# Kernel tuning notes

Hardware: AMD Instinct MI355X
Metric: run time of the kernel (lower is better)

## Reference

```python
import jax, jax.numpy as jnp
import numpy as np
from jax import lax

D_MODEL, D_STATE, D_CONV, EXPAND = 1024, 16, 4, 2
D_INNER = EXPAND * D_MODEL
B_SZ, L_SEQ = 2, 2048

# BitLinear quantization (BitNet b1.58 style, STE via stop_gradient)

def _weight_quant(w):
    scale = jnp.maximum(jnp.mean(jnp.abs(w)), 1e-5)
    q = jnp.clip(jnp.round(w / scale), -1.0, 1.0) * scale
    return w + lax.stop_gradient(q - w)

def _act_quant(x):
    s = 127.0 / jnp.maximum(jnp.max(jnp.abs(x), axis=-1, keepdims=True), 1e-5)
    q = jnp.clip(jnp.round(x * s), -128.0, 127.0) / s
    return x + lax.stop_gradient(q - x)

def bitlinear(x, w, b=None):
    y = _act_quant(x) @ _weight_quant(w).T
    return y + b if b is not None else y


def setup_inputs() -> dict:
    key = jax.random.key(0)
    ks = jax.random.split(key, 9)
    inp = {
        "x": jax.random.normal(ks[0], (B_SZ, L_SEQ, D_MODEL), jnp.float32),
        "in_proj_w": jax.random.normal(ks[1], (2 * D_INNER, D_MODEL), jnp.float32) * 0.02,
        "conv_w": jax.random.normal(ks[2], (D_INNER, 1, D_CONV), jnp.float32) * 0.2,
        "conv_b": jnp.zeros((D_INNER,), jnp.float32),
        "delta_w": jax.random.normal(ks[3], (D_STATE, D_INNER), jnp.float32) * 0.02,
        "delta_b": jnp.zeros((D_STATE,), jnp.float32),
        "B_w": jax.random.normal(ks[4], (D_STATE, D_INNER), jnp.float32) * 0.02,
        "C_w": jax.random.normal(ks[5], (D_STATE, D_INNER), jnp.float32) * 0.02,
        "out_w": jax.random.normal(ks[6], (D_MODEL, D_INNER), jnp.float32) * 0.02,
        "D": jnp.ones((D_INNER,), jnp.float32),
        "log_A": -0.5 * jnp.log(1.0 + jnp.arange(1, D_STATE + 1, dtype=jnp.float32) / D_STATE),
    }
    return inp


def reference(x, in_proj_w, conv_w, conv_b, delta_w, delta_b, B_w, C_w, out_w, D, log_A):
    B, L, _ = x.shape
    # input projection + SiLU gating
    xp = bitlinear(x, in_proj_w)                      # [B, L, 2*d_inner]
    x_gate, x_input = jnp.split(xp, 2, axis=-1)
    x_input = jax.nn.silu(x_gate) * x_input          # [B, L, d_inner]
    # causal depthwise conv1d (padding d_conv-1 then truncation == left-pad)
    xc = lax.conv_general_dilated(
        x_input.transpose(0, 2, 1), conv_w, window_strides=(1,),
        padding=[(D_CONV - 1, 0)], feature_group_count=D_INNER)
    x_input = (xc + conv_b[None, :, None]).transpose(0, 2, 1)  # [B, L, d_inner]
    # selective parameters
    delta = bitlinear(x_input, delta_w, delta_b)     # [B, L, N]
    A_d = jnp.exp(delta * log_A[None, None, :])      # [B, L, N]
    B_mat = bitlinear(x_input, B_w)                  # [B, L, N]
    C_mat = bitlinear(x_input, C_w)                  # [B, L, N]
    # diagonal state recurrence via lax.scan over time
    dB = delta * B_mat                               # [B, L, N]
    def step(h, ins):
        a_t, db_t, c_t = ins                         # each [B, N]
        h = a_t * h + db_t
        return h, jnp.sum(c_t * h, axis=-1)          # signal: [B]
    h0 = jnp.zeros((B, D_STATE), x.dtype)
    _, sig = lax.scan(step, h0, (A_d.transpose(1, 0, 2), dB.transpose(1, 0, 2), C_mat.transpose(1, 0, 2)))
    state_signal = sig.T[:, :, None]                 # [B, L, 1]
    y_inner = x_input * (jax.nn.sigmoid(state_signal) + D[None, None, :])
    return bitlinear(y_inner, out_w)                 # [B, L, d_model]
```

## Files before the change

### kernel.cpp

```cpp
#include <hip/hip_runtime.h>
#include <hip/hip_bf16.h>

typedef signed char i8;
typedef int v4i __attribute__((ext_vector_type(4)));

#define LSTR 80

__device__ __forceinline__ void gld16(const void* g, void* l) {
  __builtin_amdgcn_global_load_lds(
      (const __attribute__((address_space(1))) unsigned int*)g,
      (__attribute__((address_space(3))) unsigned int*)l, 16, 0, 0);
}

__global__ __launch_bounds__(256) void k_abssum_all(const float* __restrict__ w0, const float* __restrict__ w1,
                                                    const float* __restrict__ w2, const float* __restrict__ w3,
                                                    const float* __restrict__ w4, double* __restrict__ partial) {
  int b = blockIdx.x;
  const float* w; int n, nb, bg;
  if (b < 256)      { w = w0; n = 4194304; nb = 256; bg = b; }
  else if (b < 272) { w = w1; n = 32768;   nb = 16;  bg = b - 256; }
  else if (b < 288) { w = w2; n = 32768;   nb = 16;  bg = b - 272; }
  else if (b < 304) { w = w3; n = 32768;   nb = 16;  bg = b - 288; }
  else              { w = w4; n = 2097152; nb = 128; bg = b - 304; }
  __shared__ double sd[256];
  double acc = 0.0;
  for (int i = bg * 256 + threadIdx.x; i < n; i += nb * 256) acc += (double)fabsf(w[i]);
  sd[threadIdx.x] = acc;
  __syncthreads();
  for (int s = 128; s > 0; s >>= 1) {
    if (threadIdx.x < s) sd[threadIdx.x] += sd[threadIdx.x + s];
    __syncthreads();
  }
  if (threadIdx.x == 0) partial[b] = sd[0];
}

__global__ void k_finalize(const double* __restrict__ partial, float* __restrict__ scales) {
  int m = threadIdx.x;
  if (m >= 5) return;
  const int off[6] = {0, 256, 272, 288, 304, 432};
  const double cnt[5] = {4194304.0, 32768.0, 32768.0, 32768.0, 2097152.0};
  double s = 0.0;
  for (int i = off[m]; i < off[m + 1]; ++i) s += partial[i];
  scales[m] = fmaxf((float)(s / cnt[m]), 1e-5f);
}

__global__ __launch_bounds__(256) void k_wquant_all(const float* __restrict__ w0, const float* __restrict__ w1,
                                                    const float* __restrict__ w2, const float* __restrict__ w3,
                                                    const float* __restrict__ w4, const float* __restrict__ scales,
                                                    i8* __restrict__ tin, i8* __restrict__ t2, i8* __restrict__ tout) {
  int b = blockIdx.x;
  const float* w; i8* t; int m, n;
  if (b < 4096)      { w = w0; t = tin;          m = 0; n = 4194304; }
  else if (b < 4128) { w = w1; t = t2;           m = 1; n = 32768; b -= 4096; }
  else if (b < 4160) { w = w2; t = t2 + 32768;   m = 2; n = 32768; b -= 4128; }
  else if (b < 4192) { w = w3; t = t2 + 65536;   m = 3; n = 32768; b -= 4160; }
  else               { w = w4; t = tout;         m = 4; n = 2097152; b -= 4192; }
  int idx = (b * 256 + threadIdx.x) * 4;
  if (idx >= n) return;
  float scale = scales[m];
  float4 v = *(const float4*)(w + idx);
  char4 q;
  q.x = (i8)fminf(fmaxf(rintf(v.x / scale), -1.f), 1.f);
  q.y = (i8)fminf(fmaxf(rintf(v.y / scale), -1.f), 1.f);
  q.z = (i8)fminf(fmaxf(rintf(v.z / scale), -1.f), 1.f);
  q.w = (i8)fminf(fmaxf(rintf(v.w / scale), -1.f), 1.f);
  *(char4*)(t + idx) = q;
}

template <int W>
__global__ __launch_bounds__(256) void k_actquant(const float* __restrict__ x,
                                                  i8* __restrict__ q, float* __restrict__ srow) {
  constexpr int E = W / 256;
  const int r = blockIdx.x, tid = threadIdx.x;
  const float* xr = x + (size_t)r * W;
  float v[E];
  float m = 0.f;
#pragma unroll
  for (int j = 0; j < E; j += 4) {
    float4 t = *(const float4*)(xr + tid * E + j);
    v[j] = t.x; v[j + 1] = t.y; v[j + 2] = t.z; v[j + 3] = t.w;
    m = fmaxf(m, fmaxf(fmaxf(fabsf(t.x), fabsf(t.y)), fmaxf(fabsf(t.z), fabsf(t.w))));
  }
  __shared__ float sm[4];
  __shared__ float sbc;
#pragma unroll
  for (int off = 32; off > 0; off >>= 1) m = fmaxf(m, __shfl_xor(m, off));
  if ((tid & 63) == 0) sm[tid >> 6] = m;
  __syncthreads();
  if (tid == 0) {
    float mm = fmaxf(fmaxf(sm[0], sm[1]), fmaxf(sm[2], sm[3]));
    float s = 127.0f / fmaxf(mm, 1e-5f);
    sbc = s;
    srow[r] = s;
  }
  __syncthreads();
  float s = sbc;
#pragma unroll
  for (int j = 0; j < E; j += 4) {
    char4 c;
    c.x = (i8)fminf(fmaxf(rintf(v[j] * s), -128.f), 127.f);
    c.y = (i8)fminf(fmaxf(rintf(v[j + 1] * s), -128.f), 127.f);
    c.z = (i8)fminf(fmaxf(rintf(v[j + 2] * s), -128.f), 127.f);
    c.w = (i8)fminf(fmaxf(rintf(v[j + 3] * s), -128.f), 127.f);
    *(char4*)(q + (size_t)r * W + tid * E + j) = c;
  }
}

__global__ __launch_bounds__(256) void k_gemm1(const i8* __restrict__ qx, const i8* __restrict__ tin,
                                               const float* __restrict__ sx, const float* __restrict__ scales,
                                               float* __restrict__ gated) {
  __shared__ i8 As[16384], Bg[16384], Bv[16384];
  __shared__ float frow[128];
  const int tid = threadIdx.x;
  const int r0 = blockIdx.x * 128, c0 = blockIdx.y * 128;
  if (tid < 128) frow[tid] = scales[0] / sx[r0 + tid];
  const int lane = tid & 63, wv = tid >> 6;
  const int wr = wv >> 1, wc = wv & 1;
  const int lo = lane & 15, hi = lane >> 4;
  const int sr = tid >> 3;
  const int sp = tid & 7;
  v4i accg[4][4], accv[4][4];
#pragma unroll
  for (int m = 0; m < 4; ++m)
#pragma unroll
    for (int n = 0; n < 4; ++n) {
      accg[m][n] = (v4i){0, 0, 0, 0};
      accv[m][n] = (v4i){0, 0, 0, 0};
    }
  for (int kt = 0; kt < 8; ++kt) {
    const int kb = kt * 128;
    __syncthreads();
#pragma unroll
    for (int i = 0; i < 4; ++i) {
      int r = i * 32 + sr;
      int src = kb + ((sp ^ (r & 7)) << 4);
      int lds = i * 4096 + wv * 1024;
      gld16(qx + (size_t)(r0 + r) * 1024 + src, As + lds);
      gld16(tin + (size_t)(c0 + r) * 1024 + src, Bg + lds);
      gld16(tin + (size_t)(2048 + c0 + r) * 1024 + src, Bv + lds);
    }
    __syncthreads();
#pragma unroll
    for (int kh = 0; kh < 2; ++kh) {
      v4i a[4];
#pragma unroll
      for (int m = 0; m < 4; ++m) {
        int rr = wr * 64 + m * 16 + lo;
        int c = kh * 4 + hi;
        a[m] = *(const v4i*)&As[rr * 128 + ((c ^ (rr & 7)) << 4)];
      }
#pragma unroll
      for (int n = 0; n < 4; ++n) {
        int cc = wc * 64 + n * 16 + lo;
        int c = kh * 4 + hi;
        int off = cc * 128 + ((c ^ (cc & 7)) << 4);
        v4i bg = *(const v4i*)&Bg[off];
        v4i bv = *(const v4i*)&Bv[off];
#pragma unroll
        for (int m = 0; m < 4; ++m) {
          accg[m][n] = __builtin_amdgcn_mfma_i32_16x16x64_i8(a[m], bg, accg[m][n], 0, 0, 0);
          accv[m][n] = __builtin_amdgcn_mfma_i32_16x16x64_i8(a[m], bv, accv[m][n], 0, 0, 0);
        }
      }
    }
  }
#pragma unroll
  for (int m = 0; m < 4; ++m)
#pragma unroll
    for (int n = 0; n < 4; ++n)
#pragma unroll
      for (int rg = 0; rg < 4; ++rg) {
        int row = wr * 64 + m * 16 + hi * 4 + rg;
        int col = wc * 64 + n * 16 + lo;
        float f = frow[row];
        float g = (float)accg[m][n][rg] * f;
        float v = (float)accv[m][n][rg] * f;
        float sg = 1.0f / (1.0f + expf(-g));
        gated[(size_t)(r0 + row) * 2048 + c0 + col] = g * sg * v;
      }
}

__global__ __launch_bounds__(256) void k_convq(const float* __restrict__ g, const float* __restrict__ cw,
                                               const float* __restrict__ cb, float* __restrict__ xo,
                                               i8* __restrict__ q, float* __restrict__ srow) {
  const int tid = threadIdx.x;
  const int r0 = blockIdx.x * 8;
  const int l0 = r0 & 2047;
  const int ch = tid * 8;
  const int lane = tid & 63, wv = tid >> 6;
  float wt[4][8];
#pragma unroll
  for (int j = 0; j < 8; ++j) {
    float4 w = *(const float4*)(cw + (ch + j) * 4);
    wt[0][j] = w.x; wt[1][j] = w.y; wt[2][j] = w.z; wt[3][j] = w.w;
  }
  float bias[8];
  {
    float4 b0 = *(const float4*)(cb + ch), b1 = *(const float4*)(cb + ch + 4);
    bias[0] = b0.x; bias[1] = b0.y; bias[2] = b0.z; bias[3] = b0.w;
    bias[4] = b1.x; bias[5] = b1.y; bias[6] = b1.z; bias[7] = b1.w;
  }
  const float* gb = g + (size_t)r0 * 2048 + ch;
  float wm3[8], wm2[8], wm1[8];
  if (l0 != 0) {
    float4 a, b;
    a = *(const float4*)(gb - 3 * 2048); b = *(const float4*)(gb - 3 * 2048 + 4);
    wm3[0]=a.x; wm3[1]=a.y; wm3[2]=a.z; wm3[3]=a.w; wm3[4]=b.x; wm3[5]=b.y; wm3[6]=b.z; wm3[7]=b.w;
    a = *(const float4*)(gb - 2 * 2048); b = *(const float4*)(gb - 2 * 2048 + 4);
    wm2[0]=a.x; wm2[1]=a.y; wm2[2]=a.z; wm2[3]=a.w; wm2[4]=b.x; wm2[5]=b.y; wm2[6]=b.z; wm2[7]=b.w;
    a = *(const float4*)(gb - 1 * 2048); b = *(const float4*)(gb - 1 * 2048 + 4);
    wm1[0]=a.x; wm1[1]=a.y; wm1[2]=a.z; wm1[3]=a.w; wm1[4]=b.x; wm1[5]=b.y; wm1[6]=b.z; wm1[7]=b.w;
  } else {
#pragma unroll
    for (int j = 0; j < 8; ++j) { wm3[j] = 0.f; wm2[j] = 0.f; wm1[j] = 0.f; }
  }
  float* xop = xo + (size_t)r0 * 2048 + ch;
  float rowmax[8];
#pragma unroll
  for (int l = 0; l < 8; ++l) {
    float cur[8];
    {
      float4 a = *(const float4*)(gb + l * 2048), b = *(const float4*)(gb + l * 2048 + 4);
      cur[0]=a.x; cur[1]=a.y; cur[2]=a.z; cur[3]=a.w; cur[4]=b.x; cur[5]=b.y; cur[6]=b.z; cur[7]=b.w;
    }
    float acc[8];
    float m = 0.f;
#pragma unroll
    for (int j = 0; j < 8; ++j) {
      float v = bias[j];
      v = fmaf(wt[0][j], wm3[j], v);
      v = fmaf(wt[1][j], wm2[j], v);
      v = fmaf(wt[2][j], wm1[j], v);
      v = fmaf(wt[3][j], cur[j], v);
      acc[j] = v;
      m = fmaxf(m, fabsf(v));
    }
    rowmax[l] = m;
    *(float4*)(xop + l * 2048) = make_float4(acc[0], acc[1], acc[2], acc[3]);
    *(float4*)(xop + l * 2048 + 4) = make_float4(acc[4], acc[5], acc[6], acc[7]);
#pragma unroll
    for (int j = 0; j < 8; ++j) { wm3[j] = wm2[j]; wm2[j] = wm1[j]; wm1[j] = cur[j]; }
  }
  __shared__ float sred[8][4];
  __shared__ float sscale[8];
#pragma unroll
  for (int l = 0; l < 8; ++l) {
    float m = rowmax[l];
#pragma unroll
    for (int off = 32; off > 0; off >>= 1) m = fmaxf(m, __shfl_xor(m, off));
    if (lane == 0) sred[l][wv] = m;
  }
  __syncthreads();
  if (tid < 8) {
    float mm = fmaxf(fmaxf(sred[tid][0], sred[tid][1]), fmaxf(sred[tid][2], sred[tid][3]));
    float s = 127.0f / fmaxf(mm, 1e-5f);
    sscale[tid] = s;
    srow[r0 + tid] = s;
  }
  __syncthreads();
  i8* qp = q + (size_t)r0 * 2048 + ch;
#pragma unroll
  for (int l = 0; l < 8; ++l) {
    float s = sscale[l];
    float4 a = *(const float4*)(xop + l * 2048);
    float4 b = *(const float4*)(xop + l * 2048 + 4);
    char4 c0q, c1q;
    c0q.x = (i8)fminf(fmaxf(rintf(a.x * s), -128.f), 127.f);
    c0q.y = (i8)fminf(fmaxf(rintf(a.y * s), -128.f), 127.f);
    c0q.z = (i8)fminf(fmaxf(rintf(a.z * s), -128.f), 127.f);
    c0q.w = (i8)fminf(fmaxf(rintf(a.w * s), -128.f), 127.f);
    c1q.x = (i8)fminf(fmaxf(rintf(b.x * s), -128.f), 127.f);
    c1q.y = (i8)fminf(fmaxf(rintf(b.y * s), -128.f), 127.f);
    c1q.z = (i8)fminf(fmaxf(rintf(b.z * s), -128.f), 127.f);
    c1q.w = (i8)fminf(fmaxf(rintf(b.w * s), -128.f), 127.f);
    *(char4*)(qp + l * 2048) = c0q;
    *(char4*)(qp + l * 2048 + 4) = c1q;
  }
}

__global__ __launch_bounds__(256) void k_gemm2(const i8* __restrict__ q2, const i8* __restrict__ t2,
                                               int* __restrict__ ipart) {
  __shared__ i8 As[64 * LSTR];
  __shared__ i8 Bs[48 * LSTR];
  const int tid = threadIdx.x;
  const int r0 = blockIdx.x * 64;
  const int kb = blockIdx.y * 1024;
  const int lrow = tid >> 2, lk = (tid & 3) * 16;
  const int lane = tid & 63, wv = tid >> 6;
  const int fr = lane & 15, fk = (lane >> 4) * 16;
  v4i acc[3];
#pragma unroll
  for (int s = 0; s < 3; ++s) acc[s] = (v4i){0, 0, 0, 0};
  for (int ks = 0; ks < 16; ++ks) {
    const int k0 = kb + ks * 64;
    __syncthreads();
    *(v4i*)&As[lrow * LSTR + lk] = *(const v4i*)&q2[(size_t)(r0 + lrow) * 2048 + k0 + lk];
    if (tid < 192)
      *(v4i*)&Bs[(tid >> 2) * LSTR + (tid & 3) * 16] = *(const v4i*)&t2[(size_t)(tid >> 2) * 2048 + k0 + (tid & 3) * 16];
    __syncthreads();
    v4i a = *(const v4i*)&As[(wv * 16 + fr) * LSTR + fk];
#pragma unroll
    for (int s = 0; s < 3; ++s) {
      v4i b = *(const v4i*)&Bs[(s * 16 + fr) * LSTR + fk];
      acc[s] = __builtin_amdgcn_mfma_i32_16x16x64_i8(a, b, acc[s], 0, 0, 0);
    }
  }
#pragma unroll
  for (int s = 0; s < 3; ++s)
#pragma unroll
    for (int rg = 0; rg < 4; ++rg) {
      int row = wv * 16 + (lane >> 4) * 4 + rg;
      int col = s * 16 + (lane & 15);
      ipart[(size_t)blockIdx.y * 196608 + (size_t)(r0 + row) * 48 + col] = acc[s][rg];
    }
}

__global__ __launch_bounds__(256) void k_xform(const int* __restrict__ ip, const float* __restrict__ s2,
                                               const float* __restrict__ scales, const float* __restrict__ dbias,
                                               const float* __restrict__ logA, float* __restrict__ At,
                                               float* __restrict__ dBt, float* __restrict__ Ct) {
  int idx = blockIdx.x * 256 + threadIdx.x;
  int r = idx >> 4, n = idx & 15;
  int b = r >> 11, l = r & 2047;
  float fr = 1.0f / s2[r];
  int base = r * 48;
  float dd = (float)(ip[base + n] + ip[196608 + base + n]) * (scales[1] * fr) + dbias[n];
  float Bv = (float)(ip[base + 16 + n] + ip[196608 + base + 16 + n]) * (scales[2] * fr);
  float Cv = (float)(ip[base + 32 + n] + ip[196608 + base + 32 + n]) * (scales[3] * fr);
  int o = ((b * 16 + n) << 11) | l;
  At[o] = expf(dd * logA[n]);
  dBt[o] = dd * Bv;
  Ct[o] = Cv;
}

__global__ __launch_bounds__(256) void k_scan(const float* __restrict__ At, const float* __restrict__ dBt,
                                              const float* __restrict__ Ct, float* __restrict__ ch) {
  const int i = threadIdx.x;
  const int base = blockIdx.x << 11;
  float a[8], db[8], c[8];
  {
    const float4* p = (const float4*)(At + base + i * 8);
    float4 t0 = p[0], t1 = p[1];
    a[0]=t0.x; a[1]=t0.y; a[2]=t0.z; a[3]=t0.w; a[4]=t1.x; a[5]=t1.y; a[6]=t1.z; a[7]=t1.w;
  }
  {
    const float4* p = (const float4*)(dBt + base + i * 8);
    float4 t0 = p[0], t1 = p[1];
    db[0]=t0.x; db[1]=t0.y; db[2]=t0.z; db[3]=t0.w; db[4]=t1.x; db[5]=t1.y; db[6]=t1.z; db[7]=t1.w;
  }
  {
    const float4* p = (const float4*)(Ct + base + i * 8);
    float4 t0 = p[0], t1 = p[1];
    c[0]=t0.x; c[1]=t0.y; c[2]=t0.z; c[3]=t0.w; c[4]=t1.x; c[5]=t1.y; c[6]=t1.z; c[7]=t1.w;
  }
  float Ac = 1.f, Bc = 0.f;
#pragma unroll
  for (int j = 0; j < 8; ++j) { Bc = a[j] * Bc + db[j]; Ac *= a[j]; }
  __shared__ float sA[256], sB[256];
  sA[i] = Ac; sB[i] = Bc;
  __syncthreads();
  for (int off = 1; off < 256; off <<= 1) {
    float pA = 1.f, pB = 0.f;
    if (i >= off) { pA = sA[i - off]; pB = sB[i - off]; }
    __syncthreads();
    Bc = Ac * pB + Bc;
    Ac = Ac * pA;
    sA[i] = Ac; sB[i] = Bc;
    __syncthreads();
  }
  float h = (i > 0) ? sB[i - 1] : 0.f;
  float o[8];
#pragma unroll
  for (int j = 0; j < 8; ++j) { h = a[j] * h + db[j]; o[j] = c[j] * h; }
  float4* po = (float4*)(ch + base + i * 8);
  po[0] = make_float4(o[0], o[1], o[2], o[3]);
  po[1] = make_float4(o[4], o[5], o[6], o[7]);
}

__global__ __launch_bounds__(256) void k_yq(const float* __restrict__ xin, const float* __restrict__ chb,
                                            const float* __restrict__ Dp, i8* __restrict__ q,
                                            float* __restrict__ srow) {
  const int tid = threadIdx.x;
  const int r0 = blockIdx.x * 8;
  const int b = r0 >> 11, l0 = r0 & 2047;
  const int lane = tid & 63, wv = tid >> 6;
  __shared__ float ssig[8 * 16];
  __shared__ float ssg[8];
  __shared__ float sred[8][4];
  __shared__ float sscale[8];
  if (tid < 128) {
    int n = tid >> 3, li = tid & 7;
    ssig[li * 16 + n] = chb[((size_t)(b * 16 + n) << 11) | (l0 + li)];
  }
  __syncthreads();
  if (tid < 8) {
    float s = 0.f;
    for (int n = 0; n < 16; ++n) s += ssig[tid * 16 + n];
    ssg[tid] = 1.0f / (1.0f + expf(-s));
  }
  __syncthreads();
  const int ch = tid * 8;
  float dreg[8];
  {
    float4 d0 = *(const float4*)(Dp + ch), d1 = *(const float4*)(Dp + ch + 4);
    dreg[0]=d0.x; dreg[1]=d0.y; dreg[2]=d0.z; dreg[3]=d0.w;
    dreg[4]=d1.x; dreg[5]=d1.y; dreg[6]=d1.z; dreg[7]=d1.w;
  }
  const float* xr = xin + (size_t)r0 * 2048 + ch;
  float rowmax[8];
#pragma unroll
  for (int l = 0; l < 8; ++l) {
    float sg = ssg[l];
    float4 a = *(const float4*)(xr + l * 2048);
    float4 c = *(const float4*)(xr + l * 2048 + 4);
    float m = 0.f;
    m = fmaxf(m, fabsf(a.x * (sg + dreg[0])));
    m = fmaxf(m, fabsf(a.y * (sg + dreg[1])));
    m = fmaxf(m, fabsf(a.z * (sg + dreg[2])));
    m = fmaxf(m, fabsf(a.w * (sg + dreg[3])));
    m = fmaxf(m, fabsf(c.x * (sg + dreg[4])));
    m = fmaxf(m, fabsf(c.y * (sg + dreg[5])));
    m = fmaxf(m, fabsf(c.z * (sg + dreg[6])));
    m = fmaxf(m, fabsf(c.w * (sg + dreg[7])));
    rowmax[l] = m;
  }
#pragma unroll
  for (int l = 0; l < 8; ++l) {
    float m = rowmax[l];
#pragma unroll
    for (int off = 32; off > 0; off >>= 1) m = fmaxf(m, __shfl_xor(m, off));
    if (lane == 0) sred[l][wv] = m;
  }
  __syncthreads();
  if (tid < 8) {
    float mm = fmaxf(fmaxf(sred[tid][0], sred[tid][1]), fmaxf(sred[tid][2], sred[tid][3]));
    float s = 127.0f / fmaxf(mm, 1e-5f);
    sscale[tid] = s;
    srow[r0 + tid] = s;
  }
  __syncthreads();
  i8* qp = q + (size_t)r0 * 2048 + ch;
#pragma unroll
  for (int l = 0; l < 8; ++l) {
    float s = sscale[l];
    float sg = ssg[l];
    float4 a = *(const float4*)(xr + l * 2048);
    float4 c = *(const float4*)(xr + l * 2048 + 4);
    char4 c0q, c1q;
    c0q.x = (i8)fminf(fmaxf(rintf(a.x * (sg + dreg[0]) * s), -128.f), 127.f);
    c0q.y = (i8)fminf(fmaxf(rintf(a.y * (sg + dreg[1]) * s), -128.f), 127.f);
    c0q.z = (i8)fminf(fmaxf(rintf(a.z * (sg + dreg[2]) * s), -128.f), 127.f);
    c0q.w = (i8)fminf(fmaxf(rintf(a.w * (sg + dreg[3]) * s), -128.f), 127.f);
    c1q.x = (i8)fminf(fmaxf(rintf(c.x * (sg + dreg[4]) * s), -128.f), 127.f);
    c1q.y = (i8)fminf(fmaxf(rintf(c.y * (sg + dreg[5]) * s), -128.f), 127.f);
    c1q.z = (i8)fminf(fmaxf(rintf(c.z * (sg + dreg[6]) * s), -128.f), 127.f);
    c1q.w = (i8)fminf(fmaxf(rintf(c.w * (sg + dreg[7]) * s), -128.f), 127.f);
    *(char4*)(qp + l * 2048) = c0q;
    *(char4*)(qp + l * 2048 + 4) = c1q;
  }
}

__global__ __launch_bounds__(256) void k_gemm3(const i8* __restrict__ q3, const i8* __restrict__ tout,
                                               const float* __restrict__ s3, const float* __restrict__ scales,
                                               float* __restrict__ out) {
  __shared__ i8 As[16384], Bs[16384];
  __shared__ float frow[128];
  const int tid = threadIdx.x;
  const int r0 = blockIdx.x * 128, c0 = blockIdx.y * 128;
  if (tid < 128) frow[tid] = scales[4] / s3[r0 + tid];
  const int lane = tid & 63, wv = tid >> 6;
  const int wr = wv >> 1, wc = wv & 1;
  const int lo = lane & 15, hi = lane >> 4;
  const int sr = tid >> 3;
  const int sp = tid & 7;
  v4i acc[4][4];
#pragma unroll
  for (int m = 0; m < 4; ++m)
#pragma unroll
    for (int n = 0; n < 4; ++n) acc[m][n] = (v4i){0, 0, 0, 0};
  for (int kt = 0; kt < 16; ++kt) {
    const int kb = kt * 128;
    __syncthreads();
#pragma unroll
    for (int i = 0; i < 4; ++i) {
      int r = i * 32 + sr;
      int src = kb + ((sp ^ (r & 7)) << 4);
      int lds = i * 4096 + wv * 1024;
      gld16(q3 + (size_t)(r0 + r) * 2048 + src, As + lds);
      gld16(tout + (size_t)(c0 + r) * 2048 + src, Bs + lds);
    }
    __syncthreads();
#pragma unroll
    for (int kh = 0; kh < 2; ++kh) {
      v4i a[4];
#pragma unroll
      for (int m = 0; m < 4; ++m) {
        int rr = wr * 64 + m * 16 + lo;
        int c = kh * 4 + hi;
        a[m] = *(const v4i*)&As[rr * 128 + ((c ^ (rr & 7)) << 4)];
      }
#pragma unroll
      for (int n = 0; n < 4; ++n) {
        int cc = wc * 64 + n * 16 + lo;
        int c = kh * 4 + hi;
        v4i b = *(const v4i*)&Bs[cc * 128 + ((c ^ (cc & 7)) << 4)];
#pragma unroll
        for (int m = 0; m < 4; ++m)
          acc[m][n] = __builtin_amdgcn_mfma_i32_16x16x64_i8(a[m], b, acc[m][n], 0, 0, 0);
      }
    }
  }
#pragma unroll
  for (int m = 0; m < 4; ++m)
#pragma unroll
    for (int n = 0; n < 4; ++n)
#pragma unroll
      for (int rg = 0; rg < 4; ++rg) {
        int row = wr * 64 + m * 16 + hi * 4 + rg;
        int col = wc * 64 + n * 16 + lo;
        out[(size_t)(r0 + row) * 1024 + c0 + col] = (float)acc[m][n][rg] * frow[row];
      }
}

extern "C" void kernel_launch(void* const* d_in, const int* in_sizes, int n_in,
                              void* d_out, int out_size, void* d_ws, size_t ws_size,
                              hipStream_t stream) {
  const float* x     = (const float*)d_in[0];
  const float* win   = (const float*)d_in[1];
  const float* cw    = (const float*)d_in[2];
  const float* cb    = (const float*)d_in[3];
  const float* dw    = (const float*)d_in[4];
  const float* dbias = (const float*)d_in[5];
  const float* bw    = (const float*)d_in[6];
  const float* cmw   = (const float*)d_in[7];
  const float* ow    = (const float*)d_in[8];
  const float* Dp    = (const float*)d_in[9];
  const float* logA  = (const float*)d_in[10];
  float* out = (float*)d_out;

  char* p = (char*)d_ws;
  float* gated = (float*)p;   p += (size_t)4096 * 2048 * 4;
  float* xin   = (float*)p;   p += (size_t)4096 * 2048 * 4;
  char* qx_rgn = p;           p += (size_t)4096 * 1024;
  char* tin_rgn = p;          p += (size_t)2 * 2048 * 1024;
  i8* tout = (i8*)p;          p += (size_t)1024 * 2048;
  i8* t2   = (i8*)p;          p += (size_t)48 * 2048;
  i8* q2   = (i8*)p;          p += (size_t)4096 * 2048;
  i8* q3   = (i8*)p;          p += (size_t)4096 * 2048;
  float* sx  = (float*)p;     p += (size_t)4096 * 4;
  float* s2  = (float*)p;     p += (size_t)4096 * 4;
  float* s3  = (float*)p;     p += (size_t)4096 * 4;
  float* scales = (float*)p;  p += 256;
  double* partial = (double*)p;

  i8* qx  = (i8*)qx_rgn;
  i8* tin = (i8*)tin_rgn;
  int* ipart = (int*)qx_rgn;
  float* At  = (float*)tin_rgn;
  float* dBt = At + 65536;
  float* Ct  = dBt + 65536;
  float* chb = Ct + 65536;

  k_abssum_all<<<432, 256, 0, stream>>>(win, dw, bw, cmw, ow, partial);
  k_finalize<<<1, 64, 0, stream>>>(partial, scales);
  k_wquant_all<<<6240, 256, 0, stream>>>(win, dw, bw, cmw, ow, scales, tin, t2, tout);

  k_actquant<1024><<<4096, 256, 0, stream>>>(x, qx, sx);
  k_gemm1<<<dim3(32, 16), 256, 0, stream>>>(qx, tin, sx, scales, gated);
  k_convq<<<512, 256, 0, stream>>>(gated, cw, cb, xin, q2, s2);
  k_gemm2<<<dim3(64, 2), 256, 0, stream>>>(q2, t2, ipart);
  k_xform<<<256, 256, 0, stream>>>(ipart, s2, scales, dbias, logA, At, dBt, Ct);
  k_scan<<<32, 256, 0, stream>>>(At, dBt, Ct, chb);
  k_yq<<<512, 256, 0, stream>>>(xin, chb, Dp, q3, s3);
  k_gemm3<<<dim3(32, 8), 256, 0, stream>>>(q3, tout, s3, scales, out);
}
```

Baseline: 163.6 us.

## Load GEMM fragments directly from global into registers, drop LDS staging

The two large int8 GEMMs stop staging tiles through LDS with global_load_lds and barriers. Each wave now loads its MFMA fragments straight from global memory with a register double-buffer. Blocks grow to 512 threads (gemm1 tiles 256 rows, gemm3 keeps 128 rows with smaller per-wave tiles). Separately, convq and yq keep computed values in registers instead of re-reading from global for the quantization pass. This removes LDS traffic and synchronization, but the fragment loads are only 16 bytes per lane with strided rows, and each operand tile is loaded by several waves with no sharing through LDS, so L2 traffic goes up.

```diff
diff --git a/kernel.cpp b/kernel.cpp
--- a/kernel.cpp
+++ b/kernel.cpp
@@ -5,12 +5,7 @@
 typedef int v4i __attribute__((ext_vector_type(4)));
 
 #define LSTR 80
-
-__device__ __forceinline__ void gld16(const void* g, void* l) {
-  __builtin_amdgcn_global_load_lds(
-      (const __attribute__((address_space(1))) unsigned int*)g,
-      (__attribute__((address_space(3))) unsigned int*)l, 16, 0, 0);
-}
+#define MFMA_I8 __builtin_amdgcn_mfma_i32_16x16x64_i8
 
 __global__ __launch_bounds__(256) void k_abssum_all(const float* __restrict__ w0, const float* __restrict__ w1,
                                                     const float* __restrict__ w2, const float* __restrict__ w3,
@@ -106,19 +101,25 @@
   }
 }
 
-__global__ __launch_bounds__(256) void k_gemm1(const i8* __restrict__ qx, const i8* __restrict__ tin,
+__global__ __launch_bounds__(512) void k_gemm1(const i8* __restrict__ qx, const i8* __restrict__ tin,
                                                const float* __restrict__ sx, const float* __restrict__ scales,
                                                float* __restrict__ gated) {
-  __shared__ i8 As[16384], Bg[16384], Bv[16384];
-  __shared__ float frow[128];
+  __shared__ float frow[256];
   const int tid = threadIdx.x;
-  const int r0 = blockIdx.x * 128, c0 = blockIdx.y * 128;
-  if (tid < 128) frow[tid] = scales[0] / sx[r0 + tid];
+  const int r0 = blockIdx.x * 256, c0 = blockIdx.y * 128;
+  if (tid < 256) frow[tid] = scales[0] / sx[r0 + tid];
+  __syncthreads();
   const int lane = tid & 63, wv = tid >> 6;
-  const int wr = wv >> 1, wc = wv & 1;
+  const int wm = wv >> 1, wn = wv & 1;
   const int lo = lane & 15, hi = lane >> 4;
-  const int sr = tid >> 3;
-  const int sp = tid & 7;
+  int offA[4], offG[4], offV[4];
+#pragma unroll
+  for (int m = 0; m < 4; ++m) offA[m] = (r0 + wm * 64 + m * 16 + lo) * 1024 + hi * 16;
+#pragma unroll
+  for (int n = 0; n < 4; ++n) {
+    offG[n] = (c0 + wn * 64 + n * 16 + lo) * 1024 + hi * 16;
+    offV[n] = (2048 + c0 + wn * 64 + n * 16 + lo) * 1024 + hi * 16;
+  }
   v4i accg[4][4], accv[4][4];
 #pragma unroll
   for (int m = 0; m < 4; ++m)
@@ -127,51 +128,45 @@
       accg[m][n] = (v4i){0, 0, 0, 0};
       accv[m][n] = (v4i){0, 0, 0, 0};
     }
-  for (int kt = 0; kt < 8; ++kt) {
-    const int kb = kt * 128;
-    __syncthreads();
-#pragma unroll
-    for (int i = 0; i < 4; ++i) {
-      int r = i * 32 + sr;
-      int src = kb + ((sp ^ (r & 7)) << 4);
-      int lds = i * 4096 + wv * 1024;
-      gld16(qx + (size_t)(r0 + r) * 1024 + src, As + lds);
-      gld16(tin + (size_t)(c0 + r) * 1024 + src, Bg + lds);
-      gld16(tin + (size_t)(2048 + c0 + r) * 1024 + src, Bv + lds);
-    }
-    __syncthreads();
-#pragma unroll
-    for (int kh = 0; kh < 2; ++kh) {
-      v4i a[4];
-#pragma unroll
-      for (int m = 0; m < 4; ++m) {
-        int rr = wr * 64 + m * 16 + lo;
-        int c = kh * 4 + hi;
-        a[m] = *(const v4i*)&As[rr * 128 + ((c ^ (rr & 7)) << 4)];
-      }
-#pragma unroll
-      for (int n = 0; n < 4; ++n) {
-        int cc = wc * 64 + n * 16 + lo;
-        int c = kh * 4 + hi;
-        int off = cc * 128 + ((c ^ (cc & 7)) << 4);
-        v4i bg = *(const v4i*)&Bg[off];
-        v4i bv = *(const v4i*)&Bv[off];
-#pragma unroll
-        for (int m = 0; m < 4; ++m) {
-          accg[m][n] = __builtin_amdgcn_mfma_i32_16x16x64_i8(a[m], bg, accg[m][n], 0, 0, 0);
-          accv[m][n] = __builtin_amdgcn_mfma_i32_16x16x64_i8(a[m], bv, accv[m][n], 0, 0, 0);
-        }
-      }
-    }
-  }
+  v4i a0[4], g0[4], v0[4], a1[4], g1[4], v1[4];
+
+#define LD1(t, A, G, V)                                                         \
+  {                                                                             \
+    _Pragma("unroll") for (int m = 0; m < 4; ++m)                               \
+        A[m] = *(const v4i*)(qx + offA[m] + (t) * 64);                          \
+    _Pragma("unroll") for (int n = 0; n < 4; ++n) {                             \
+      G[n] = *(const v4i*)(tin + offG[n] + (t) * 64);                           \
+      V[n] = *(const v4i*)(tin + offV[n] + (t) * 64);                           \
+    }                                                                           \
+  }
+#define FM1(A, G, V)                                                            \
+  {                                                                             \
+    _Pragma("unroll") for (int n = 0; n < 4; ++n)                               \
+        _Pragma("unroll") for (int m = 0; m < 4; ++m) {                         \
+      accg[m][n] = MFMA_I8(A[m], G[n], accg[m][n], 0, 0, 0);                    \
+      accv[m][n] = MFMA_I8(A[m], V[n], accv[m][n], 0, 0, 0);                    \
+    }                                                                           \
+  }
+
+  LD1(0, a0, g0, v0);
+#pragma unroll
+  for (int t = 0; t < 16; t += 2) {
+    if (t + 1 < 16) LD1(t + 1, a1, g1, v1);
+    FM1(a0, g0, v0);
+    if (t + 2 < 16) LD1(t + 2, a0, g0, v0);
+    if (t + 1 < 16) FM1(a1, g1, v1);
+  }
+#undef LD1
+#undef FM1
+
 #pragma unroll
   for (int m = 0; m < 4; ++m)
 #pragma unroll
     for (int n = 0; n < 4; ++n)
 #pragma unroll
       for (int rg = 0; rg < 4; ++rg) {
-        int row = wr * 64 + m * 16 + hi * 4 + rg;
-        int col = wc * 64 + n * 16 + lo;
+        int row = wm * 64 + m * 16 + hi * 4 + rg;
+        int col = wn * 64 + n * 16 + lo;
         float f = frow[row];
         float g = (float)accg[m][n][rg] * f;
         float v = (float)accv[m][n][rg] * f;
@@ -215,6 +210,7 @@
     for (int j = 0; j < 8; ++j) { wm3[j] = 0.f; wm2[j] = 0.f; wm1[j] = 0.f; }
   }
   float* xop = xo + (size_t)r0 * 2048 + ch;
+  float y[8][8];
   float rowmax[8];
 #pragma unroll
   for (int l = 0; l < 8; ++l) {
@@ -223,7 +219,6 @@
       float4 a = *(const float4*)(gb + l * 2048), b = *(const float4*)(gb + l * 2048 + 4);
       cur[0]=a.x; cur[1]=a.y; cur[2]=a.z; cur[3]=a.w; cur[4]=b.x; cur[5]=b.y; cur[6]=b.z; cur[7]=b.w;
     }
-    float acc[8];
     float m = 0.f;
 #pragma unroll
     for (int j = 0; j < 8; ++j) {
@@ -232,12 +227,12 @@
       v = fmaf(wt[1][j], wm2[j], v);
       v = fmaf(wt[2][j], wm1[j], v);
       v = fmaf(wt[3][j], cur[j], v);
-      acc[j] = v;
+      y[l][j] = v;
       m = fmaxf(m, fabsf(v));
     }
     rowmax[l] = m;
-    *(float4*)(xop + l * 2048) = make_float4(acc[0], acc[1], acc[2], acc[3]);
-    *(float4*)(xop + l * 2048 + 4) = make_float4(acc[4], acc[5], acc[6], acc[7]);
+    *(float4*)(xop + l * 2048) = make_float4(y[l][0], y[l][1], y[l][2], y[l][3]);
+    *(float4*)(xop + l * 2048 + 4) = make_float4(y[l][4], y[l][5], y[l][6], y[l][7]);
 #pragma unroll
     for (int j = 0; j < 8; ++j) { wm3[j] = wm2[j]; wm2[j] = wm1[j]; wm1[j] = cur[j]; }
   }
@@ -262,17 +257,15 @@
 #pragma unroll
   for (int l = 0; l < 8; ++l) {
     float s = sscale[l];
-    float4 a = *(const float4*)(xop + l * 2048);
-    float4 b = *(const float4*)(xop + l * 2048 + 4);
     char4 c0q, c1q;
-    c0q.x = (i8)fminf(fmaxf(rintf(a.x * s), -128.f), 127.f);
-    c0q.y = (i8)fminf(fmaxf(rintf(a.y * s), -128.f), 127.f);
-    c0q.z = (i8)fminf(fmaxf(rintf(a.z * s), -128.f), 127.f);
-    c0q.w = (i8)fminf(fmaxf(rintf(a.w * s), -128.f), 127.f);
-    c1q.x = (i8)fminf(fmaxf(rintf(b.x * s), -128.f), 127.f);
-    c1q.y = (i8)fminf(fmaxf(rintf(b.y * s), -128.f), 127.f);
-    c1q.z = (i8)fminf(fmaxf(rintf(b.z * s), -128.f), 127.f);
-    c1q.w = (i8)fminf(fmaxf(rintf(b.w * s), -128.f), 127.f);
+    c0q.x = (i8)fminf(fmaxf(rintf(y[l][0] * s), -128.f), 127.f);
+    c0q.y = (i8)fminf(fmaxf(rintf(y[l][1] * s), -128.f), 127.f);
+    c0q.z = (i8)fminf(fmaxf(rintf(y[l][2] * s), -128.f), 127.f);
+    c0q.w = (i8)fminf(fmaxf(rintf(y[l][3] * s), -128.f), 127.f);
+    c1q.x = (i8)fminf(fmaxf(rintf(y[l][4] * s), -128.f), 127.f);
+    c1q.y = (i8)fminf(fmaxf(rintf(y[l][5] * s), -128.f), 127.f);
+    c1q.z = (i8)fminf(fmaxf(rintf(y[l][6] * s), -128.f), 127.f);
+    c1q.w = (i8)fminf(fmaxf(rintf(y[l][7] * s), -128.f), 127.f);
     *(char4*)(qp + l * 2048) = c0q;
     *(char4*)(qp + l * 2048 + 4) = c1q;
   }
@@ -302,7 +295,7 @@
 #pragma unroll
     for (int s = 0; s < 3; ++s) {
       v4i b = *(const v4i*)&Bs[(s * 16 + fr) * LSTR + fk];
-      acc[s] = __builtin_amdgcn_mfma_i32_16x16x64_i8(a, b, acc[s], 0, 0, 0);
+      acc[s] = MFMA_I8(a, b, acc[s], 0, 0, 0);
     }
   }
 #pragma unroll
@@ -407,21 +400,24 @@
     dreg[4]=d1.x; dreg[5]=d1.y; dreg[6]=d1.z; dreg[7]=d1.w;
   }
   const float* xr = xin + (size_t)r0 * 2048 + ch;
+  float y[8][8];
   float rowmax[8];
 #pragma unroll
   for (int l = 0; l < 8; ++l) {
     float sg = ssg[l];
     float4 a = *(const float4*)(xr + l * 2048);
     float4 c = *(const float4*)(xr + l * 2048 + 4);
+    y[l][0] = a.x * (sg + dreg[0]);
+    y[l][1] = a.y * (sg + dreg[1]);
+    y[l][2] = a.z * (sg + dreg[2]);
+    y[l][3] = a.w * (sg + dreg[3]);
+    y[l][4] = c.x * (sg + dreg[4]);
+    y[l][5] = c.y * (sg + dreg[5]);
+    y[l][6] = c.z * (sg + dreg[6]);
+    y[l][7] = c.w * (sg + dreg[7]);
     float m = 0.f;
-    m = fmaxf(m, fabsf(a.x * (sg + dreg[0])));
-    m = fmaxf(m, fabsf(a.y * (sg + dreg[1])));
-    m = fmaxf(m, fabsf(a.z * (sg + dreg[2])));
-    m = fmaxf(m, fabsf(a.w * (sg + dreg[3])));
-    m = fmaxf(m, fabsf(c.x * (sg + dreg[4])));
-    m = fmaxf(m, fabsf(c.y * (sg + dreg[5])));
-    m = fmaxf(m, fabsf(c.z * (sg + dreg[6])));
-    m = fmaxf(m, fabsf(c.w * (sg + dreg[7])));
+#pragma unroll
+    for (int j = 0; j < 8; ++j) m = fmaxf(m, fabsf(y[l][j]));
     rowmax[l] = m;
   }
 #pragma unroll
@@ -443,81 +439,76 @@
 #pragma unroll
   for (int l = 0; l < 8; ++l) {
     float s = sscale[l];
-    float sg = ssg[l];
-    float4 a = *(const float4*)(xr + l * 2048);
-    float4 c = *(const float4*)(xr + l * 2048 + 4);
     char4 c0q, c1q;
-    c0q.x = (i8)fminf(fmaxf(rintf(a.x * (sg + dreg[0]) * s), -128.f), 127.f);
-    c0q.y = (i8)fminf(fmaxf(rintf(a.y * (sg + dreg[1]) * s), -128.f), 127.f);
-    c0q.z = (i8)fminf(fmaxf(rintf(a.z * (sg + dreg[2]) * s), -128.f), 127.f);
-    c0q.w = (i8)fminf(fmaxf(rintf(a.w * (sg + dreg[3]) * s), -128.f), 127.f);
-    c1q.x = (i8)fminf(fmaxf(rintf(c.x * (sg + dreg[4]) * s), -128.f), 127.f);
-    c1q.y = (i8)fminf(fmaxf(rintf(c.y * (sg + dreg[5]) * s), -128.f), 127.f);
-    c1q.z = (i8)fminf(fmaxf(rintf(c.z * (sg + dreg[6]) * s), -128.f), 127.f);
-    c1q.w = (i8)fminf(fmaxf(rintf(c.w * (sg + dreg[7]) * s), -128.f), 127.f);
+    c0q.x = (i8)fminf(fmaxf(rintf(y[l][0] * s), -128.f), 127.f);
+    c0q.y = (i8)fminf(fmaxf(rintf(y[l][1] * s), -128.f), 127.f);
+    c0q.z = (i8)fminf(fmaxf(rintf(y[l][2] * s), -128.f), 127.f);
+    c0q.w = (i8)fminf(fmaxf(rintf(y[l][3] * s), -128.f), 127.f);
+    c1q.x = (i8)fminf(fmaxf(rintf(y[l][4] * s), -128.f), 127.f);
+    c1q.y = (i8)fminf(fmaxf(rintf(y[l][5] * s), -128.f), 127.f);
+    c1q.z = (i8)fminf(fmaxf(rintf(y[l][6] * s), -128.f), 127.f);
+    c1q.w = (i8)fminf(fmaxf(rintf(y[l][7] * s), -128.f), 127.f);
     *(char4*)(qp + l * 2048) = c0q;
     *(char4*)(qp + l * 2048 + 4) = c1q;
   }
 }
 
-__global__ __launch_bounds__(256) void k_gemm3(const i8* __restrict__ q3, const i8* __restrict__ tout,
+__global__ __launch_bounds__(512) void k_gemm3(const i8* __restrict__ q3, const i8* __restrict__ tout,
                                                const float* __restrict__ s3, const float* __restrict__ scales,
                                                float* __restrict__ out) {
-  __shared__ i8 As[16384], Bs[16384];
   __shared__ float frow[128];
   const int tid = threadIdx.x;
   const int r0 = blockIdx.x * 128, c0 = blockIdx.y * 128;
   if (tid < 128) frow[tid] = scales[4] / s3[r0 + tid];
+  __syncthreads();
   const int lane = tid & 63, wv = tid >> 6;
-  const int wr = wv >> 1, wc = wv & 1;
+  const int wm = wv >> 1, wn = wv & 1;
   const int lo = lane & 15, hi = lane >> 4;
-  const int sr = tid >> 3;
-  const int sp = tid & 7;
-  v4i acc[4][4];
-#pragma unroll
-  for (int m = 0; m < 4; ++m)
+  int offA[2], offB[4];
+#pragma unroll
+  for (int m = 0; m < 2; ++m) offA[m] = (r0 + wm * 32 + m * 16 + lo) * 2048 + hi * 16;
+#pragma unroll
+  for (int n = 0; n < 4; ++n) offB[n] = (c0 + wn * 64 + n * 16 + lo) * 2048 + hi * 16;
+  v4i acc[2][4];
+#pragma unroll
+  for (int m = 0; m < 2; ++m)
 #pragma unroll
     for (int n = 0; n < 4; ++n) acc[m][n] = (v4i){0, 0, 0, 0};
-  for (int kt = 0; kt < 16; ++kt) {
-    const int kb = kt * 128;
-    __syncthreads();
-#pragma unroll
-    for (int i = 0; i < 4; ++i) {
-      int r = i * 32 + sr;
-      int src = kb + ((sp ^ (r & 7)) << 4);
-      int lds = i * 4096 + wv * 1024;
-      gld16(q3 + (size_t)(r0 + r) * 2048 + src, As + lds);
-      gld16(tout + (size_t)(c0 + r) * 2048 + src, Bs + lds);
-    }
-    __syncthreads();
-#pragma unroll
-    for (int kh = 0; kh < 2; ++kh) {
-      v4i a[4];
-#pragma unroll
-      for (int m = 0; m < 4; ++m) {
-        int rr = wr * 64 + m * 16 + lo;
-        int c = kh * 4 + hi;
-        a[m] = *(const v4i*)&As[rr * 128 + ((c ^ (rr & 7)) << 4)];
-      }
-#pragma unroll
-      for (int n = 0; n < 4; ++n) {
-        int cc = wc * 64 + n * 16 + lo;
-        int c = kh * 4 + hi;
-        v4i b = *(const v4i*)&Bs[cc * 128 + ((c ^ (cc & 7)) << 4)];
-#pragma unroll
-        for (int m = 0; m < 4; ++m)
-          acc[m][n] = __builtin_amdgcn_mfma_i32_16x16x64_i8(a[m], b, acc[m][n], 0, 0, 0);
-      }
-    }
-  }
-#pragma unroll
-  for (int m = 0; m < 4; ++m)
+  v4i a0[2], b0[4], a1[2], b1[4];
+
+#define LD3(t, A, B)                                                            \
+  {                                                                             \
+    _Pragma("unroll") for (int m = 0; m < 2; ++m)                               \
+        A[m] = *(const v4i*)(q3 + offA[m] + (t) * 64);                          \
+    _Pragma("unroll") for (int n = 0; n < 4; ++n)                               \
+        B[n] = *(const v4i*)(tout + offB[n] + (t) * 64);                        \
+  }
+#define FM3(A, B)                                                               \
+  {                                                                             \
+    _Pragma("unroll") for (int n = 0; n < 4; ++n)                               \
+        _Pragma("unroll") for (int m = 0; m < 2; ++m)                           \
+            acc[m][n] = MFMA_I8(A[m], B[n], acc[m][n], 0, 0, 0);                \
+  }
+
+  LD3(0, a0, b0);
+#pragma unroll
+  for (int t = 0; t < 32; t += 2) {
+    if (t + 1 < 32) LD3(t + 1, a1, b1);
+    FM3(a0, b0);
+    if (t + 2 < 32) LD3(t + 2, a0, b0);
+    if (t + 1 < 32) FM3(a1, b1);
+  }
+#undef LD3
+#undef FM3
+
+#pragma unroll
+  for (int m = 0; m < 2; ++m)
 #pragma unroll
     for (int n = 0; n < 4; ++n)
 #pragma unroll
       for (int rg = 0; rg < 4; ++rg) {
-        int row = wr * 64 + m * 16 + hi * 4 + rg;
-        int col = wc * 64 + n * 16 + lo;
+        int row = wm * 32 + m * 16 + hi * 4 + rg;
+        int col = wn * 64 + n * 16 + lo;
         out[(size_t)(r0 + row) * 1024 + c0 + col] = (float)acc[m][n][rg] * frow[row];
       }
 }
@@ -566,11 +557,11 @@
   k_wquant_all<<<6240, 256, 0, stream>>>(win, dw, bw, cmw, ow, scales, tin, t2, tout);
 
   k_actquant<1024><<<4096, 256, 0, stream>>>(x, qx, sx);
-  k_gemm1<<<dim3(32, 16), 256, 0, stream>>>(qx, tin, sx, scales, gated);
+  k_gemm1<<<dim3(16, 16), 512, 0, stream>>>(qx, tin, sx, scales, gated);
   k_convq<<<512, 256, 0, stream>>>(gated, cw, cb, xin, q2, s2);
   k_gemm2<<<dim3(64, 2), 256, 0, stream>>>(q2, t2, ipart);
   k_xform<<<256, 256, 0, stream>>>(ipart, s2, scales, dbias, logA, At, dBt, Ct);
   k_scan<<<32, 256, 0, stream>>>(At, dBt, Ct, chb);
   k_yq<<<512, 256, 0, stream>>>(xin, chb, Dp, q3, s3);
-  k_gemm3<<<dim3(32, 8), 256, 0, stream>>>(q3, tout, s3, scales, out);
-}
+  k_gemm3<<<dim3(32, 8), 512, 0, stream>>>(q3, tout, s3, scales, out);
+}
```

New measurement: 205.7 us. 1.26x slower.
